# Optimization experiments

Hardware: AMD Instinct MI355X
Metric: run time of the kernel (lower is better)

The kernel has to match this reference:

```python
import jax, jax.numpy as jnp
import numpy as np

N_HEADS = 16
ROPE_BASE = 10000.0


def apply_rope(x):
    # x: [B, H, T, D]; rotate interleaved pairs along last dim, positions along T
    B, H, T, D = x.shape
    half = D // 2
    inv_freq = 1.0 / (ROPE_BASE ** (jnp.arange(0, half, dtype=jnp.float32) * 2.0 / D))
    angles = jnp.arange(T, dtype=jnp.float32)[:, None] * inv_freq[None, :]  # [T, half]
    cos = jnp.cos(angles).astype(x.dtype)  # [T, half]
    sin = jnp.sin(angles).astype(x.dtype)
    xp = x.reshape(B, H, T, half, 2)
    x1, x2 = xp[..., 0], xp[..., 1]
    out = jnp.stack([x1 * cos - x2 * sin, x1 * sin + x2 * cos], axis=-1)
    return out.reshape(B, H, T, D)


def setup_inputs() -> dict:
    key = jax.random.key(0)
    k1, k2, k3 = jax.random.split(key, 3)
    C = 1024
    x = jax.random.normal(k1, (2, 2048, C), dtype=jnp.float32)
    w_qkv = jax.random.normal(k2, (C, 3 * C), dtype=jnp.float32) * (1.0 / np.sqrt(C))
    w_out = jax.random.normal(k3, (C, C), dtype=jnp.float32) * (1.0 / np.sqrt(C))
    return {"x": x, "w_qkv": w_qkv, "w_out": w_out}


def reference(x, w_qkv, w_out):
    B, T, C = x.shape
    H = N_HEADS
    D = C // H
    qkv = (x @ w_qkv).reshape(B, T, 3, H, D)
    q, k, v = qkv[:, :, 0], qkv[:, :, 1], qkv[:, :, 2]  # [B, T, H, D]
    q = jnp.transpose(q, (0, 2, 1, 3))  # [B, H, T, D]
    k = jnp.transpose(k, (0, 2, 1, 3))
    v = jnp.transpose(v, (0, 2, 1, 3))
    q = apply_rope(q)
    k = apply_rope(k)
    scale = 1.0 / np.sqrt(D)
    scores = jnp.einsum('bhqd,bhkd->bhqk', q, k) * scale
    causal = jnp.tril(jnp.ones((T, T), dtype=bool))
    scores = jnp.where(causal, scores, jnp.finfo(scores.dtype).min)
    attn = jax.nn.softmax(scores, axis=-1)
    out = jnp.einsum('bhqk,bhkd->bhqd', attn, v)  # [B, H, T, D]
    out = jnp.transpose(out, (0, 2, 1, 3)).reshape(B, T, C)
    return out @ w_out
```

## Files before the change

### kernel.cpp

```cpp
#include <hip/hip_runtime.h>
#include <hip/hip_bf16.h>

typedef __attribute__((ext_vector_type(8))) short v8s;
typedef __attribute__((ext_vector_type(4))) float v4f;
typedef __attribute__((ext_vector_type(16))) float v16f;

typedef const __attribute__((address_space(1))) void* gas_ptr;
typedef __attribute__((address_space(3))) void* las_ptr;

#define MFMA16(a, b, c) __builtin_amdgcn_mfma_f32_16x16x32_bf16((a), (b), (c), 0, 0, 0)
#define MFMA32(a, b, c) __builtin_amdgcn_mfma_f32_32x32x16_bf16((a), (b), (c), 0, 0, 0)

__device__ __forceinline__ void gload_lds16(const void* g, void* l) {
  __builtin_amdgcn_global_load_lds((gas_ptr)g, (las_ptr)l, 16, 0, 0);
}

__device__ __forceinline__ unsigned short f2bf(float f) {
  unsigned int u = __float_as_uint(f);
  u += 0x7FFFu + ((u >> 16) & 1u);
  return (unsigned short)(u >> 16);
}
__device__ __forceinline__ float bf2f(unsigned short h) {
  return __uint_as_float(((unsigned int)h) << 16);
}

__device__ __forceinline__ unsigned cvt_pk_bf16(float lo, float hi) {
  unsigned r;
  asm("v_cvt_pk_bf16_f32 %0, %1, %2" : "=v"(r) : "v"(lo), "v"(hi));
  return r;
}

__global__ __launch_bounds__(256) void k_convert(const float* __restrict__ in,
                                                 unsigned short* __restrict__ out, int n4) {
  int i = blockIdx.x * 256 + threadIdx.x;
  if (i >= n4) return;
  float4 v = ((const float4*)in)[i];
  ushort4 o;
  o.x = f2bf(v.x); o.y = f2bf(v.y); o.z = f2bf(v.z); o.w = f2bf(v.w);
  ((ushort4*)out)[i] = o;
}

__global__ __launch_bounds__(256) void k_transpose_convert(const float* __restrict__ in,
                                                           unsigned short* __restrict__ out,
                                                           int R, int C) {
  __shared__ __attribute__((aligned(16))) unsigned short tb[64 * 72];
  const int r0 = blockIdx.y * 64, c0 = blockIdx.x * 64;
  const int tid = threadIdx.x;
#pragma unroll
  for (int j = 0; j < 4; ++j) {
    int slot = tid + 256 * j;
    int row = slot >> 4, q4 = (slot & 15) * 4;
    float4 v = *(const float4*)&in[(size_t)(r0 + row) * C + c0 + q4];
    ushort4 o;
    o.x = f2bf(v.x); o.y = f2bf(v.y); o.z = f2bf(v.z); o.w = f2bf(v.w);
    *(ushort4*)&tb[row * 72 + q4] = o;
  }
  __syncthreads();
#pragma unroll
  for (int j = 0; j < 4; ++j) {
    int slot = tid + 256 * j;
    int crow = slot >> 4, t4 = (slot & 15) * 4;
    ushort4 o;
    o.x = tb[(t4 + 0) * 72 + crow];
    o.y = tb[(t4 + 1) * 72 + crow];
    o.z = tb[(t4 + 2) * 72 + crow];
    o.w = tb[(t4 + 3) * 72 + crow];
    *(ushort4*)&out[(size_t)(c0 + crow) * R + r0 + t4] = o;
  }
}

template <bool F32OUT>
__global__ __launch_bounds__(256) void k_gemm(const unsigned short* __restrict__ A,
                                              const unsigned short* __restrict__ Bt,
                                              void* __restrict__ Cout,
                                              int M, int N, int K) {
  __shared__ __attribute__((aligned(16))) unsigned short As[128 * 32];
  __shared__ __attribute__((aligned(16))) unsigned short Bs[128 * 32];
  const int tid = threadIdx.x;
  const int w = tid >> 6, l = tid & 63, g = l >> 4, c = l & 15;
  const int wr = w >> 1, wc = w & 1;
  const int mt = blockIdx.y * 128, nt = blockIdx.x * 128;
  const int rowc = l >> 2, kslot = (l & 3) * 8;

  v4f acc[4][4];
#pragma unroll
  for (int m = 0; m < 4; ++m)
#pragma unroll
    for (int n = 0; n < 4; ++n) acc[m][n] = (v4f){0.f, 0.f, 0.f, 0.f};

  for (int kt = 0; kt < K; kt += 32) {
    __syncthreads();
#pragma unroll
    for (int i = 0; i < 2; ++i) {
      int ch = w + 4 * i;
      gload_lds16(&A[(size_t)(mt + ch * 16 + rowc) * K + kt + kslot], &As[ch * 512]);
      gload_lds16(&Bt[(size_t)(nt + ch * 16 + rowc) * K + kt + kslot], &Bs[ch * 512]);
    }
    __syncthreads();
    v8s af[4], bfr[4];
#pragma unroll
    for (int m = 0; m < 4; ++m)
      af[m] = *(const v8s*)&As[(wr * 64 + m * 16 + c) * 32 + g * 8];
#pragma unroll
    for (int n = 0; n < 4; ++n)
      bfr[n] = *(const v8s*)&Bs[(wc * 64 + n * 16 + c) * 32 + g * 8];
#pragma unroll
    for (int m = 0; m < 4; ++m)
#pragma unroll
      for (int n = 0; n < 4; ++n)
        acc[m][n] = MFMA16(af[m], bfr[n], acc[m][n]);
  }

#pragma unroll
  for (int m = 0; m < 4; ++m)
#pragma unroll
    for (int n = 0; n < 4; ++n)
#pragma unroll
      for (int r = 0; r < 4; ++r) {
        int row = mt + wr * 64 + m * 16 + g * 4 + r;
        int col = nt + wc * 64 + n * 16 + c;
        if (F32OUT)
          ((float*)Cout)[(size_t)row * N + col] = acc[m][n][r];
        else
          ((unsigned short*)Cout)[(size_t)row * N + col] = f2bf(acc[m][n][r]);
      }
}

__global__ __launch_bounds__(256) void k_post(const unsigned short* __restrict__ qkv,
                                              unsigned short* __restrict__ qp,
                                              unsigned short* __restrict__ kp,
                                              unsigned short* __restrict__ vp) {
  __shared__ float2 cs[64 * 32];
  __shared__ __attribute__((aligned(16))) unsigned short vt[64 * 72];
  const int bh = blockIdx.y;
  const int b = bh >> 4, hd = bh & 15;
  const int t0 = blockIdx.x * 64;
  const int tid = threadIdx.x;

#pragma unroll
  for (int e = 0; e < 8; ++e) {
    int idx = tid + 256 * e;
    int tl = idx >> 5, i = idx & 31;
    float invf = exp2f(-(float)i * 0.41524101186092034f);
    float ang = (float)(t0 + tl) * invf;
    float s, cc;
    sincosf(ang, &s, &cc);
    cs[idx] = make_float2(cc, s);
  }
#pragma unroll
  for (int j = 0; j < 2; ++j) {
    int slot = tid + 256 * j;
    int row = slot >> 3, c8 = (slot & 7) * 8;
    v8s vv = *(const v8s*)&qkv[(size_t)(b * 2048 + t0 + row) * 3072 + 2048 + hd * 64 + c8];
    *(v8s*)&vt[row * 72 + c8] = vv;
  }
  __syncthreads();

#pragma unroll
  for (int j = 0; j < 2; ++j) {
    int slot = tid + 256 * j;
    int row = slot >> 3, d0 = (slot & 7) * 8;
    int t = t0 + row;
    size_t base = (size_t)(b * 2048 + t) * 3072 + hd * 64;
    const int tile = t >> 5, c32 = t & 31, kd = d0 >> 4, hh = (d0 >> 3) & 1;
    const size_t pidx = (size_t)bh * 131072 + (tile * 4 + kd) * 512 + (hh * 32 + c32) * 8;
#pragma unroll
    for (int which = 0; which < 2; ++which) {
      const float qsc = which ? 1.0f : 0.18033688011112042f;
      v8s vq = *(const v8s*)&qkv[base + which * 1024 + d0];
      union { unsigned short s[8]; v8s v; } uo;
#pragma unroll
      for (int p = 0; p < 4; ++p) {
        float2 sc = cs[row * 32 + d0 / 2 + p];
        float x1 = bf2f((unsigned short)vq[2 * p]);
        float x2 = bf2f((unsigned short)vq[2 * p + 1]);
        uo.s[2 * p]     = f2bf((x1 * sc.x - x2 * sc.y) * qsc);
        uo.s[2 * p + 1] = f2bf((x1 * sc.y + x2 * sc.x) * qsc);
      }
      unsigned short* dst = which ? kp : qp;
      *(v8s*)&dst[pidx] = uo.v;
    }
  }

#pragma unroll
  for (int jj = 0; jj < 2; ++jj) {
    int idx = tid + 256 * jj;
    int tl = idx >> 8, kc = (idx >> 7) & 1, md = (idx >> 6) & 1;
    int lp = idx & 63, hh = lp >> 5, c32 = lp & 31;
    int d = md * 32 + c32;
    int brow = tl * 32 + kc * 16 + hh * 4;
    union { unsigned short s[8]; v8s v; } uo;
#pragma unroll
    for (int jh = 0; jh < 2; ++jh)
#pragma unroll
      for (int e = 0; e < 4; ++e)
        uo.s[jh * 4 + e] = vt[(brow + jh * 8 + e) * 72 + d];
    int tileG = (t0 >> 5) + tl;
    *(v8s*)&vp[(size_t)bh * 131072 + ((tileG * 2 + kc) * 2 + md) * 512 + lp * 8] = uo.v;
  }
}

__global__ __launch_bounds__(64) void k_attn(const unsigned short* __restrict__ qp,
                                             const unsigned short* __restrict__ kp,
                                             const unsigned short* __restrict__ vp,
                                             unsigned short* __restrict__ ao,
                                             char* __restrict__ part) {
  const int bh = blockIdx.y;
  const int idx = 159 - (int)blockIdx.x;
  int j, s;
  if (idx >= 96)      { j = 48 + ((idx - 96) >> 2); s = (idx - 96) & 3; }
  else if (idx >= 48) { j = 32 + (idx - 48) / 3;    s = (idx - 48) % 3; }
  else if (idx >= 16) { j = 16 + ((idx - 16) >> 1); s = (idx - 16) & 1; }
  else                { j = idx;                    s = 0; }
  const int t0 = s * 16;
  const int t1 = (t0 + 16 < j + 1) ? (t0 + 16) : (j + 1);

  const int l = threadIdx.x;
  const int c32 = l & 31, hh = l >> 5;
  const unsigned short* Qb = qp + (size_t)bh * 131072 + j * 4 * 512;
  const unsigned short* Kb = kp + (size_t)bh * 131072;
  const unsigned short* Vb = vp + (size_t)bh * 131072;

  v8s bq[4];
#pragma unroll
  for (int kd = 0; kd < 4; ++kd) bq[kd] = *(const v8s*)&Qb[kd * 512 + l * 8];

  v16f ot[2] = {{0,0,0,0,0,0,0,0,0,0,0,0,0,0,0,0},
                {0,0,0,0,0,0,0,0,0,0,0,0,0,0,0,0}};
  float m2 = -1e30f, ls = 0.f;

  v8s ak[4], av[2][2];
#pragma unroll
  for (int kd = 0; kd < 4; ++kd) ak[kd] = *(const v8s*)&Kb[(t0 * 4 + kd) * 512 + l * 8];
#pragma unroll
  for (int kc = 0; kc < 2; ++kc)
#pragma unroll
    for (int md = 0; md < 2; ++md)
      av[kc][md] = *(const v8s*)&Vb[((t0 * 2 + kc) * 2 + md) * 512 + l * 8];

  for (int t = t0; t < t1; ++t) {
    v16f st = {0,0,0,0,0,0,0,0,0,0,0,0,0,0,0,0};
#pragma unroll
    for (int kd = 0; kd < 4; ++kd) st = MFMA32(ak[kd], bq[kd], st);

    if (t + 1 < t1) {
#pragma unroll
      for (int kd = 0; kd < 4; ++kd)
        ak[kd] = *(const v8s*)&Kb[((t + 1) * 4 + kd) * 512 + l * 8];
    }

    if (t == j) {
#pragma unroll
      for (int r = 0; r < 16; ++r) {
        int rloc = (r & 3) + 8 * (r >> 2) + 4 * hh;
        st[r] = (rloc <= c32) ? st[r] : -1e30f;
      }
    }

    float a0 = fmaxf(st[0], st[1]),   a1 = fmaxf(st[2], st[3]);
    float a2 = fmaxf(st[4], st[5]),   a3 = fmaxf(st[6], st[7]);
    float a4 = fmaxf(st[8], st[9]),   a5 = fmaxf(st[10], st[11]);
    float a6 = fmaxf(st[12], st[13]), a7 = fmaxf(st[14], st[15]);
    float b0m = fmaxf(fmaxf(a0, a1), fmaxf(a2, a3));
    float b1m = fmaxf(fmaxf(a4, a5), fmaxf(a6, a7));
    float pm = fmaxf(b0m, b1m);
    pm = fmaxf(pm, __shfl_xor(pm, 32));
    if (!__all(pm <= m2 + 8.f)) {
      float mn = fmaxf(m2, pm);
      float al = exp2f(m2 - mn);
      m2 = mn;
      ls *= al;
      ot[0] *= al;
      ot[1] *= al;
    }
    float rs = 0.f;
#pragma unroll
    for (int r = 0; r < 16; ++r) {
      float p = exp2f(st[r] - m2);
      st[r] = p;
      rs += p;
    }
    rs += __shfl_xor(rs, 32);
    ls += rs;

    unsigned wd[8];
#pragma unroll
    for (int i = 0; i < 8; ++i) wd[i] = cvt_pk_bf16(st[2 * i], st[2 * i + 1]);
    union { unsigned u[4]; v8s v; } pb0, pb1;
    pb0.u[0] = wd[0]; pb0.u[1] = wd[1]; pb0.u[2] = wd[2]; pb0.u[3] = wd[3];
    pb1.u[0] = wd[4]; pb1.u[1] = wd[5]; pb1.u[2] = wd[6]; pb1.u[3] = wd[7];

    ot[0] = MFMA32(av[0][0], pb0.v, ot[0]);
    ot[1] = MFMA32(av[0][1], pb0.v, ot[1]);
    ot[0] = MFMA32(av[1][0], pb1.v, ot[0]);
    ot[1] = MFMA32(av[1][1], pb1.v, ot[1]);

    if (t + 1 < t1) {
#pragma unroll
      for (int kc = 0; kc < 2; ++kc)
#pragma unroll
        for (int md = 0; md < 2; ++md)
          av[kc][md] = *(const v8s*)&Vb[(((t + 1) * 2 + kc) * 2 + md) * 512 + l * 8];
    }
  }

  const float inv = 1.f / ls;
  if (j < 16) {
    const int b = bh >> 4, hd = bh & 15;
    const int t = j * 32 + c32;
    unsigned short* aop = ao + (size_t)(b * 2048 + t) * 1024 + hd * 64;
#pragma unroll
    for (int md = 0; md < 2; ++md)
#pragma unroll
      for (int q = 0; q < 4; ++q) {
        unsigned w0 = cvt_pk_bf16(ot[md][4 * q + 0] * inv, ot[md][4 * q + 1] * inv);
        unsigned w1 = cvt_pk_bf16(ot[md][4 * q + 2] * inv, ot[md][4 * q + 3] * inv);
        int d = md * 32 + 8 * q + 4 * hh;
        *(uint2*)&aop[d] = make_uint2(w0, w1);
      }
  } else {
    char* slot = part + ((size_t)bh * 160 + idx) * 4352;
#pragma unroll
    for (int md = 0; md < 2; ++md)
#pragma unroll
      for (int i = 0; i < 8; ++i) {
        union { _Float16 h[2]; unsigned u; } pk;
        pk.h[0] = (_Float16)(ot[md][2 * i] * inv);
        pk.h[1] = (_Float16)(ot[md][2 * i + 1] * inv);
        *(unsigned*)(slot + ((md * 8 + i) * 64 + l) * 4) = pk.u;
      }
    if (hh == 0) {
      *(float*)(slot + 4096 + c32 * 4) = m2;
      *(float*)(slot + 4224 + c32 * 4) = ls;
    }
  }
}

__global__ __launch_bounds__(64) void k_comb(const char* __restrict__ part,
                                             unsigned short* __restrict__ ao) {
  const int bh = blockIdx.y;
  const int j = 16 + (int)blockIdx.x;
  const int g = j >> 4;
  const int nch = g + 1;
  const int l = threadIdx.x, c32 = l & 31, hh = l >> 5;
  const int baseg = (g == 1) ? 16 : (g == 2) ? 48 : 96;
  const int ord0 = baseg + (j - 16 * g) * nch;
  const char* base = part + (size_t)bh * 160 * 4352;

  float ms[4], lsv[4], wsc[4];
  float mfin = -1e30f;
#pragma unroll
  for (int s = 0; s < 4; ++s) {
    if (s < nch) {
      const char* sl = base + (size_t)(ord0 + s) * 4352;
      ms[s] = *(const float*)(sl + 4096 + c32 * 4);
      lsv[s] = *(const float*)(sl + 4224 + c32 * 4);
      mfin = fmaxf(mfin, ms[s]);
    }
  }
  float lfin = 0.f;
#pragma unroll
  for (int s = 0; s < 4; ++s) {
    if (s < nch) {
      wsc[s] = lsv[s] * exp2f(ms[s] - mfin);
      lfin += wsc[s];
    }
  }
  const float inv = 1.f / lfin;
#pragma unroll
  for (int s = 0; s < 4; ++s)
    if (s < nch) wsc[s] *= inv;

  const int b = bh >> 4, hd = bh & 15;
  const int t = j * 32 + c32;
  unsigned short* aop = ao + (size_t)(b * 2048 + t) * 1024 + hd * 64;
#pragma unroll
  for (int md = 0; md < 2; ++md)
#pragma unroll
    for (int q4 = 0; q4 < 4; ++q4) {
      const int w0 = md * 8 + 2 * q4;
      float a0 = 0.f, a1 = 0.f, a2 = 0.f, a3 = 0.f;
#pragma unroll
      for (int s = 0; s < 4; ++s) {
        if (s < nch) {
          const char* sl = base + (size_t)(ord0 + s) * 4352;
          unsigned u0 = *(const unsigned*)(sl + ((w0 + 0) * 64 + l) * 4);
          unsigned u1 = *(const unsigned*)(sl + ((w0 + 1) * 64 + l) * 4);
          union { unsigned u; _Float16 h[2]; } p0, p1;
          p0.u = u0; p1.u = u1;
          a0 += (float)p0.h[0] * wsc[s];
          a1 += (float)p0.h[1] * wsc[s];
          a2 += (float)p1.h[0] * wsc[s];
          a3 += (float)p1.h[1] * wsc[s];
        }
      }
      unsigned o0 = cvt_pk_bf16(a0, a1);
      unsigned o1 = cvt_pk_bf16(a2, a3);
      int d = md * 32 + 8 * q4 + 4 * hh;
      *(uint2*)&aop[d] = make_uint2(o0, o1);
    }
}

extern "C" void kernel_launch(void* const* d_in, const int* in_sizes, int n_in,
                              void* d_out, int out_size, void* d_ws, size_t ws_size,
                              hipStream_t stream) {
  const float* x     = (const float*)d_in[0];
  const float* w_qkv = (const float*)d_in[1];
  const float* w_out = (const float*)d_in[2];
  float* out = (float*)d_out;

  char* ws = (char*)d_ws;
  unsigned short* xbf = (unsigned short*)(ws);
  unsigned short* wqT = (unsigned short*)(ws + 8388608);
  unsigned short* woT = (unsigned short*)(ws + 14680064);
  unsigned short* qkv = (unsigned short*)(ws + 16777216);
  unsigned short* qp  = (unsigned short*)(ws + 41943040);
  unsigned short* kp  = (unsigned short*)(ws + 50331648);
  unsigned short* vp  = (unsigned short*)(ws + 58720256);
  char* part = (char*)(ws + 16777216);

  k_convert<<<4096, 256, 0, stream>>>(x, xbf, 1048576);
  k_transpose_convert<<<dim3(48, 16), 256, 0, stream>>>(w_qkv, wqT, 1024, 3072);
  k_transpose_convert<<<dim3(16, 16), 256, 0, stream>>>(w_out, woT, 1024, 1024);
  k_gemm<false><<<dim3(24, 32), 256, 0, stream>>>(xbf, wqT, qkv, 4096, 3072, 1024);
  k_post<<<dim3(32, 32), 256, 0, stream>>>(qkv, qp, kp, vp);
  k_attn<<<dim3(160, 32), 64, 0, stream>>>(qp, kp, vp, xbf , part);
  k_comb<<<dim3(48, 32), 64, 0, stream>>>(part, xbf);
  k_gemm<true><<<dim3(8, 32), 256, 0, stream>>>(xbf, woT, (void*)out, 4096, 1024, 1024);
}
```

Measured before the change: 155.6 us.

## Remap attention grid by XCD, split PV accumulators, raise MFMA priority

The attention launch is flattened to a 1D grid and remapped so all 160 blocks of a batch-head land on the same XCD, which aims to improve L2 reuse of K/V. The PV output accumulation alternates between two accumulator sets across iterations to break the serial MFMA dependency chain, and the sets are summed at the end. s_setprio is raised around the MFMA groups to favour matrix issue across co-resident waves. The trade-offs are more accumulator registers, which may lower occupancy, and a changed block ordering that affects load balance.

Measured after the change: 161.4 us. 3.7% more time.

```diff
diff --git a/kernel.cpp b/kernel.cpp
--- a/kernel.cpp
+++ b/kernel.cpp
@@ -205,8 +205,10 @@
                                              const unsigned short* __restrict__ vp,
                                              unsigned short* __restrict__ ao,
                                              char* __restrict__ part) {
-  const int bh = blockIdx.y;
-  const int idx = 159 - (int)blockIdx.x;
+  const int bid = (int)blockIdx.x;
+  const int xcd = bid & 7, s2 = bid >> 3;
+  const int bh = xcd + 8 * (s2 / 160);
+  const int idx = 159 - (s2 % 160);
   int j, s;
   if (idx >= 96)      { j = 48 + ((idx - 96) >> 2); s = (idx - 96) & 3; }
   else if (idx >= 48) { j = 32 + (idx - 48) / 3;    s = (idx - 48) % 3; }
@@ -225,8 +227,8 @@
 #pragma unroll
   for (int kd = 0; kd < 4; ++kd) bq[kd] = *(const v8s*)&Qb[kd * 512 + l * 8];
 
-  v16f ot[2] = {{0,0,0,0,0,0,0,0,0,0,0,0,0,0,0,0},
-                {0,0,0,0,0,0,0,0,0,0,0,0,0,0,0,0}};
+  v16f oa0 = {0,0,0,0,0,0,0,0,0,0,0,0,0,0,0,0}, oa1 = oa0;
+  v16f ob0 = oa0, ob1 = oa0;
   float m2 = -1e30f, ls = 0.f;
 
   v8s ak[4], av[2][2];
@@ -238,10 +240,13 @@
     for (int md = 0; md < 2; ++md)
       av[kc][md] = *(const v8s*)&Vb[((t0 * 2 + kc) * 2 + md) * 512 + l * 8];
 
+  bool par = false;
   for (int t = t0; t < t1; ++t) {
     v16f st = {0,0,0,0,0,0,0,0,0,0,0,0,0,0,0,0};
+    __builtin_amdgcn_s_setprio(1);
 #pragma unroll
     for (int kd = 0; kd < 4; ++kd) st = MFMA32(ak[kd], bq[kd], st);
+    __builtin_amdgcn_s_setprio(0);
 
     if (t + 1 < t1) {
 #pragma unroll
@@ -270,8 +275,7 @@
       float al = exp2f(m2 - mn);
       m2 = mn;
       ls *= al;
-      ot[0] *= al;
-      ot[1] *= al;
+      oa0 *= al; oa1 *= al; ob0 *= al; ob1 *= al;
     }
     float rs = 0.f;
 #pragma unroll
@@ -290,10 +294,20 @@
     pb0.u[0] = wd[0]; pb0.u[1] = wd[1]; pb0.u[2] = wd[2]; pb0.u[3] = wd[3];
     pb1.u[0] = wd[4]; pb1.u[1] = wd[5]; pb1.u[2] = wd[6]; pb1.u[3] = wd[7];
 
-    ot[0] = MFMA32(av[0][0], pb0.v, ot[0]);
-    ot[1] = MFMA32(av[0][1], pb0.v, ot[1]);
-    ot[0] = MFMA32(av[1][0], pb1.v, ot[0]);
-    ot[1] = MFMA32(av[1][1], pb1.v, ot[1]);
+    __builtin_amdgcn_s_setprio(1);
+    if (par) {
+      ob0 = MFMA32(av[0][0], pb0.v, ob0);
+      ob1 = MFMA32(av[0][1], pb0.v, ob1);
+      ob0 = MFMA32(av[1][0], pb1.v, ob0);
+      ob1 = MFMA32(av[1][1], pb1.v, ob1);
+    } else {
+      oa0 = MFMA32(av[0][0], pb0.v, oa0);
+      oa1 = MFMA32(av[0][1], pb0.v, oa1);
+      oa0 = MFMA32(av[1][0], pb1.v, oa0);
+      oa1 = MFMA32(av[1][1], pb1.v, oa1);
+    }
+    __builtin_amdgcn_s_setprio(0);
+    par = !par;
 
     if (t + 1 < t1) {
 #pragma unroll
@@ -304,6 +318,7 @@
     }
   }
 
+  v16f ot0 = oa0 + ob0, ot1 = oa1 + ob1;
   const float inv = 1.f / ls;
   if (j < 16) {
     const int b = bh >> 4, hd = bh & 15;
@@ -313,8 +328,9 @@
     for (int md = 0; md < 2; ++md)
 #pragma unroll
       for (int q = 0; q < 4; ++q) {
-        unsigned w0 = cvt_pk_bf16(ot[md][4 * q + 0] * inv, ot[md][4 * q + 1] * inv);
-        unsigned w1 = cvt_pk_bf16(ot[md][4 * q + 2] * inv, ot[md][4 * q + 3] * inv);
+        const v16f& o = md ? ot1 : ot0;
+        unsigned w0 = cvt_pk_bf16(o[4 * q + 0] * inv, o[4 * q + 1] * inv);
+        unsigned w1 = cvt_pk_bf16(o[4 * q + 2] * inv, o[4 * q + 3] * inv);
         int d = md * 32 + 8 * q + 4 * hh;
         *(uint2*)&aop[d] = make_uint2(w0, w1);
       }
@@ -324,9 +340,10 @@
     for (int md = 0; md < 2; ++md)
 #pragma unroll
       for (int i = 0; i < 8; ++i) {
+        const v16f& o = md ? ot1 : ot0;
         union { _Float16 h[2]; unsigned u; } pk;
-        pk.h[0] = (_Float16)(ot[md][2 * i] * inv);
-        pk.h[1] = (_Float16)(ot[md][2 * i + 1] * inv);
+        pk.h[0] = (_Float16)(o[2 * i] * inv);
+        pk.h[1] = (_Float16)(o[2 * i + 1] * inv);
         *(unsigned*)(slot + ((md * 8 + i) * 64 + l) * 4) = pk.u;
       }
     if (hh == 0) {
@@ -424,7 +441,7 @@
   k_transpose_convert<<<dim3(16, 16), 256, 0, stream>>>(w_out, woT, 1024, 1024);
   k_gemm<false><<<dim3(24, 32), 256, 0, stream>>>(xbf, wqT, qkv, 4096, 3072, 1024);
   k_post<<<dim3(32, 32), 256, 0, stream>>>(qkv, qp, kp, vp);
-  k_attn<<<dim3(160, 32), 64, 0, stream>>>(qp, kp, vp, xbf , part);
+  k_attn<<<5120, 64, 0, stream>>>(qp, kp, vp, xbf , part);
   k_comb<<<dim3(48, 32), 64, 0, stream>>>(part, xbf);
   k_gemm<true><<<dim3(8, 32), 256, 0, stream>>>(xbf, woT, (void*)out, 4096, 1024, 1024);
 }
```
